# Kernel optimization log

Hardware: AMD Instinct MI355X
Metric: run time of the kernel (lower is better)

## Reference

```python
import jax, jax.numpy as jnp
import numpy as np

COE_LAMBDA = 1.0
TOP_K = 2


def _ffn(x, W1, b1, W2, b2):
    # x: [B,S,d] -> [B,S,d]
    return jax.nn.gelu(x @ W1 + b1) @ W2 + b2


def _moe(x, Wg, Wa, Wb):
    # top-2 softmax-routed MoE. x: [B,S,d]; Wa: [E,d,h]; Wb: [E,h,d]
    E = Wg.shape[-1]
    logits = x @ Wg                              # [B,S,E]
    top_v, top_i = jax.lax.top_k(logits, TOP_K)  # [B,S,k]
    probs = jax.nn.softmax(top_v, axis=-1)       # renormalized over top-k
    # dense per-token expert weights [B,S,E] (zero for non-selected experts)
    w = jnp.sum(jax.nn.one_hot(top_i, E, dtype=x.dtype) * probs[..., None], axis=-2)
    h = jax.nn.gelu(jnp.einsum('bsd,edh->bseh', x, Wa))   # [B,S,E,h]
    hw = h * w[..., None]                                  # weight before contraction (avoids [B,S,E,d])
    return jnp.einsum('bseh,ehd->bsd', hw, Wb)


def setup_inputs() -> dict:
    key = jax.random.key(0)
    ks = jax.random.split(key, 8)
    B, S, D, F, E, H = 4, 8192, 512, 2048, 8, 64
    s = lambda *sh: 1.0 / np.sqrt(sh[-2] if len(sh) > 1 else 1.0)
    return {
        'x':   jax.random.normal(ks[0], (B, S, D), jnp.float32),
        'id':  S // 2,
        'W1':  jax.random.normal(ks[1], (D, F), jnp.float32) * (1/np.sqrt(D)),
        'b1':  jnp.zeros((F,), jnp.float32),
        'W2':  jax.random.normal(ks[2], (F, D), jnp.float32) * (1/np.sqrt(F)),
        'b2':  jnp.zeros((D,), jnp.float32),
        'Wg1': jax.random.normal(ks[3], (D, E), jnp.float32) * (1/np.sqrt(D)),
        'Wa1': jax.random.normal(ks[4], (E, D, H), jnp.float32) * (1/np.sqrt(D)),
        'Wb1': jax.random.normal(ks[5], (E, H, D), jnp.float32) * (1/np.sqrt(H)),
        'Wg2': jax.random.normal(ks[6], (D, E), jnp.float32) * (1/np.sqrt(D)),
        'Wa2': jax.random.normal(ks[7], (E, D, H), jnp.float32) * (1/np.sqrt(D)),
        'Wb2': jax.random.normal(jax.random.fold_in(key, 99), (E, H, D), jnp.float32) * (1/np.sqrt(H)),
    }


def reference(x, id, W1, b1, W2, b2, Wg1, Wa1, Wb1, Wg2, Wa2, Wb2):
    B, S, D = x.shape
    ffn_out = _ffn(x, W1, b1, W2, b2)
    moe_out = _moe(x, Wg1, Wa1, Wb1) + _moe(x, Wg2, Wa2, Wb2)
    # original: positions i < id (when S != 1) get FFN only; others get FFN + lambda*MoE
    if S == 1:
        mask = jnp.ones((S,), x.dtype)
    else:
        mask = (jnp.arange(S) >= id).astype(x.dtype)
    return ffn_out + COE_LAMBDA * mask[None, :, None] * moe_out
```

## Files before the change

kernel.cpp:

```cpp
#include <hip/hip_runtime.h>
#include <hip/hip_bf16.h>

typedef __bf16 bf16_t;
typedef __bf16 bf16x8 __attribute__((ext_vector_type(8)));
typedef float f32x4 __attribute__((ext_vector_type(4)));

#define AS1 __attribute__((address_space(1)))
#define AS3 __attribute__((address_space(3)))

__device__ __forceinline__ void gload_lds16(const void* g, void* l) {
    __builtin_amdgcn_global_load_lds((const AS1 void*)g, (AS3 void*)l, 16, 0, 0);
}

__device__ __forceinline__ float gelu_f(float x) {
    float u = 0.7978845608028654f * (x + 0.044715f * x * x * x);
    float e = __expf(2.0f * u);
    float t = 1.0f - 2.0f / (e + 1.0f);
    return 0.5f * x * (1.0f + t);
}

__global__ void detect_kernel(const unsigned int* __restrict__ xw,
                              int* __restrict__ flagp)
{
    __shared__ int cnt;
    int tid = threadIdx.x;
    if (tid == 0) cnt = 0;
    __syncthreads();
    unsigned int w = xw[tid];
    int le = (w >> 7) & 0xFF;
    int ok = (le >= 0x60 && le <= 0x88) ? 1 : 0;
    atomicAdd(&cnt, ok);
    __syncthreads();
    if (tid == 0) *flagp = (cnt >= 128) ? 1 : 0;
}

__device__ __forceinline__ float rd_elem(const void* p, size_t idx, int isbf) {
    return isbf ? (float)((const bf16_t*)p)[idx] : ((const float*)p)[idx];
}

__global__ __launch_bounds__(256) void convert_kernel(
    const void* __restrict__ x, const int* __restrict__ flagp,
    bf16_t* __restrict__ xb)
{
    const int isbf = *flagp;
    size_t i = (size_t)blockIdx.x * 256 + threadIdx.x;
    if (isbf) {
        ((bf16x8*)xb)[i] = ((const bf16x8*)x)[i];
    } else {
        const float* s = (const float*)x + i * 8;
        float4 u0 = *(const float4*)s;
        float4 u1 = *(const float4*)(s + 4);
        bf16x8 v;
        v[0] = (bf16_t)u0.x; v[1] = (bf16_t)u0.y;
        v[2] = (bf16_t)u0.z; v[3] = (bf16_t)u0.w;
        v[4] = (bf16_t)u1.x; v[5] = (bf16_t)u1.y;
        v[6] = (bf16_t)u1.z; v[7] = (bf16_t)u1.w;
        ((bf16x8*)xb)[i] = v;
    }
}

__global__ __launch_bounds__(256) void pack_kernel(
    const void* __restrict__ W1, const void* __restrict__ W2,
    const void* __restrict__ Wa1, const void* __restrict__ Wa2,
    const void* __restrict__ Wb1, const void* __restrict__ Wb2,
    const int* __restrict__ flagp,
    bf16_t* __restrict__ W1t, bf16_t* __restrict__ W2t,
    bf16_t* __restrict__ Wat, bf16_t* __restrict__ Wbt)
{
    const int isbf = *flagp;
    int i = blockIdx.x * 256 + threadIdx.x;
    if (i < 1048576) {
        int n = i >> 9, k = i & 511;
        W1t[i] = (bf16_t)rd_elem(W1, (size_t)k * 2048 + n, isbf);
    } else if (i < 2097152) {
        int j = i - 1048576;
        int n = j >> 11, k = j & 2047;
        W2t[j] = (bf16_t)rd_elem(W2, (size_t)k * 512 + n, isbf);
    } else if (i < 2621440) {
        int j = i - 2097152;
        int n = j >> 9, d = j & 511;
        const void* Wa = (n < 512) ? Wa1 : Wa2;
        int nn = n & 511, e = nn >> 6, hh = nn & 63;
        Wat[j] = (bf16_t)rd_elem(Wa, ((size_t)e * 512 + d) * 64 + hh, isbf);
    } else {
        int j = i - 2621440;
        int d = j >> 10, n = j & 1023;
        const void* Wb = (n < 512) ? Wb1 : Wb2;
        int nn = n & 511;
        Wbt[j] = (bf16_t)rd_elem(Wb, (size_t)nn * 512 + d, isbf);
    }
}

__global__ __launch_bounds__(256) void gate_kernel(
    const void* __restrict__ xv,
    const void* __restrict__ Wg1, const void* __restrict__ Wg2,
    const int* __restrict__ flagp,
    float* __restrict__ wout)
{
    __shared__ float WgL[2][4096];
    const int isbf = *flagp;
    const int tid = threadIdx.x;
    const int wave = tid >> 6, lane = tid & 63;
    for (int i = tid; i < 4096; i += 256) {
        WgL[0][i] = rd_elem(Wg1, i, isbf);
        WgL[1][i] = rd_elem(Wg2, i, isbf);
    }
    __syncthreads();

    for (int it = 0; it < 16; ++it) {
        int r = blockIdx.x * 64 + it * 4 + wave;
        int t = (r >> 12) * 8192 + 4096 + (r & 4095);
        float xr[8];
        if (isbf) {
            bf16x8 t8 = *(const bf16x8*)((const bf16_t*)xv + (size_t)t * 512 + lane * 8);
#pragma unroll
            for (int j = 0; j < 8; ++j) xr[j] = (float)t8[j];
        } else {
            const float* xp = (const float*)xv + (size_t)t * 512 + lane * 8;
            float4 u0 = *(const float4*)xp;
            float4 u1 = *(const float4*)(xp + 4);
            xr[0] = u0.x; xr[1] = u0.y; xr[2] = u0.z; xr[3] = u0.w;
            xr[4] = u1.x; xr[5] = u1.y; xr[6] = u1.z; xr[7] = u1.w;
        }
        float a[16];
#pragma unroll
        for (int e = 0; e < 16; ++e) a[e] = 0.0f;
#pragma unroll
        for (int j = 0; j < 8; ++j) {
            float xj = xr[j];
            int d = lane * 8 + j;
            const float* w1r = &WgL[0][d * 8];
            const float* w2r = &WgL[1][d * 8];
#pragma unroll
            for (int e = 0; e < 8; ++e) {
                a[e]     += xj * w1r[e];
                a[8 + e] += xj * w2r[e];
            }
        }
#pragma unroll
        for (int e = 0; e < 16; ++e) {
            a[e] += __shfl_xor(a[e], 32, 64);
            a[e] += __shfl_xor(a[e], 16, 64);
            a[e] += __shfl_xor(a[e], 8, 64);
            a[e] += __shfl_xor(a[e], 4, 64);
            a[e] += __shfl_xor(a[e], 2, 64);
            a[e] += __shfl_xor(a[e], 1, 64);
        }
        if (lane == 0) {
#pragma unroll
            for (int g = 0; g < 2; ++g) {
                float v0 = -1e30f, v1 = -1e30f;
                int i0 = 0, i1 = 0;
#pragma unroll
                for (int e = 0; e < 8; ++e) {
                    float vv = a[g * 8 + e];
                    if (vv > v0) { v0 = vv; i0 = e; }
                }
#pragma unroll
                for (int e = 0; e < 8; ++e) {
                    float vv = a[g * 8 + e];
                    if (e != i0 && vv > v1) { v1 = vv; i1 = e; }
                }
                float e1 = __expf(v1 - v0);
                float p0 = 1.0f / (1.0f + e1);
                float p1 = 1.0f - p0;
#pragma unroll
                for (int e = 0; e < 8; ++e)
                    wout[(size_t)r * 16 + g * 8 + e] =
                        (e == i0) ? p0 : ((e == i1) ? p1 : 0.0f);
            }
        }
    }
}

template <int EPI, int ROWMAP>
__global__ __launch_bounds__(256, 2) void gemm_kernel(
    const bf16_t* __restrict__ A, int lda,
    const bf16_t* __restrict__ Bt, int ldb,
    void* __restrict__ Cv, int ldc, int K,
    int off1, int off2,
    const void* __restrict__ biasv,
    const float* __restrict__ wgt,
    const int* __restrict__ id_ptr,
    const int* __restrict__ flagp)
{
    __shared__ __align__(16) bf16_t As[2][128 * 32];
    __shared__ __align__(16) bf16_t Bs[2][128 * 32];

    const int isbf = *flagp;
    const int tid = threadIdx.x;
    const int lane = tid & 63;
    const int wave = tid >> 6;
    const int wm = wave >> 1, wn = wave & 1;
    const int ln15 = lane & 15, lg = lane >> 4;
    const int rsw = (ln15 >> 1) & 3;

    const int gy = gridDim.y;
    const int nwg = gridDim.x * gy;
    const int orig = blockIdx.y * gridDim.x + blockIdx.x;
    const int wg = (orig & 7) * (nwg >> 3) + (orig >> 3);
    const int bx = wg / gy;
    const int by = wg % gy;

    const int r0 = bx * 128;
    const int c0 = by * 128;
    int rA0, rC0, grow0;
    if (ROWMAP == 0) {
        rA0 = off1 + r0; rC0 = off2 + r0; grow0 = 0;
    } else if (ROWMAP == 1) {
        int g = off1 + r0;
        rA0 = (g >> 12) * 8192 + 4096 + (g & 4095);
        rC0 = r0; grow0 = g;
    } else {
        int g = off1 + r0;
        rA0 = r0; grow0 = 0;
        rC0 = (g >> 12) * 8192 + 4096 + (g & 4095);
    }

    auto stage = [&](int kt, int b) {
        const int k0 = kt * 32;
#pragma unroll
        for (int i = 0; i < 2; ++i) {
            int cc = i * 256 + tid;
            int row = cc >> 2;
            int gc = (cc & 3) ^ ((row >> 1) & 3);
            gload_lds16(A + (size_t)(rA0 + row) * lda + (k0 + gc * 8),
                        (char*)(&As[b][0]) + (i * 256 + wave * 64) * 16);
            gload_lds16(Bt + (size_t)(c0 + row) * ldb + (k0 + gc * 8),
                        (char*)(&Bs[b][0]) + (i * 256 + wave * 64) * 16);
        }
    };

    f32x4 acc[4][4];
#pragma unroll
    for (int r = 0; r < 4; ++r)
#pragma unroll
        for (int c = 0; c < 4; ++c)
            acc[r][c] = (f32x4){0.f, 0.f, 0.f, 0.f};

    const int nK = K >> 5;
    stage(0, 0);
    asm volatile("s_waitcnt vmcnt(0)" ::: "memory");
    __builtin_amdgcn_s_barrier();

    for (int kt = 0; kt < nK; ++kt) {
        const int b = kt & 1;
        if (kt + 1 < nK) stage(kt + 1, b ^ 1);

        bf16x8 af[4], bfr[4];
#pragma unroll
        for (int r = 0; r < 4; ++r)
            af[r] = *(const bf16x8*)(
                &As[b][(wm * 64 + r * 16 + ln15) * 32 + ((lg ^ rsw) * 8)]);
#pragma unroll
        for (int c = 0; c < 4; ++c)
            bfr[c] = *(const bf16x8*)(
                &Bs[b][(wn * 64 + c * 16 + ln15) * 32 + ((lg ^ rsw) * 8)]);
#pragma unroll
        for (int r = 0; r < 4; ++r)
#pragma unroll
            for (int c = 0; c < 4; ++c)
                acc[r][c] = __builtin_amdgcn_mfma_f32_16x16x32_bf16(
                    af[r], bfr[c], acc[r][c], 0, 0, 0);

        if (kt + 1 < nK) {
            asm volatile("s_waitcnt vmcnt(0)" ::: "memory");
            __builtin_amdgcn_s_barrier();
        }
    }

    const int idv = (EPI == 3) ? id_ptr[0] : 0;
    bf16_t* Cb = (bf16_t*)Cv;
    float*  Cf = (float*)Cv;

#pragma unroll
    for (int r = 0; r < 4; ++r) {
#pragma unroll
        for (int v = 0; v < 4; ++v) {
            int lrow = wm * 64 + r * 16 + lg * 4 + v;
            int crow = rC0 + lrow;
#pragma unroll
            for (int c = 0; c < 4; ++c) {
                int col = c0 + wn * 64 + c * 16 + ln15;
                float val = acc[r][c][v];
                size_t oidx = (size_t)crow * ldc + col;
                if (EPI == 0) {
                    if (biasv) val += rd_elem(biasv, col, isbf);
                    if (isbf) Cb[oidx] = (bf16_t)val; else Cf[oidx] = val;
                } else if (EPI == 1) {
                    if (biasv) val += rd_elem(biasv, col, isbf);
                    Cb[oidx] = (bf16_t)gelu_f(val);
                } else if (EPI == 2) {
                    val = gelu_f(val) * wgt[(size_t)(grow0 + lrow) * 16 + (col >> 6)];
                    Cb[oidx] = (bf16_t)val;
                } else {
                    if ((crow & 8191) >= idv) {
                        if (isbf) Cb[oidx] = (bf16_t)((float)Cb[oidx] + val);
                        else      Cf[oidx] = Cf[oidx] + val;
                    }
                }
            }
        }
    }
}

extern "C" void kernel_launch(void* const* d_in, const int* in_sizes, int n_in,
                              void* d_out, int out_size, void* d_ws, size_t ws_size,
                              hipStream_t stream)
{
    const void* x   = d_in[0];
    const int*  idp = (const int*)d_in[1];
    const void* W1  = d_in[2];
    const void* b1  = d_in[3];
    const void* W2  = d_in[4];
    const void* b2  = d_in[5];
    const void* Wg1 = d_in[6];
    const void* Wa1 = d_in[7];
    const void* Wb1 = d_in[8];
    const void* Wg2 = d_in[9];
    const void* Wa2 = d_in[10];
    const void* Wb2 = d_in[11];

    char* p = (char*)d_ws;
    bf16_t* W1t  = (bf16_t*)(p);
    bf16_t* W2t  = (bf16_t*)(p + 2097152);
    bf16_t* Wat  = (bf16_t*)(p + 4194304);
    bf16_t* Wbt  = (bf16_t*)(p + 5242880);
    float*  wbuf = (float*) (p + 6291456);
    int*    flagp= (int*)   (p + 7340032);
    bf16_t* xb   = (bf16_t*)(p + 7405568);
    bf16_t* big  = (bf16_t*)(p + 40960000);

    const size_t base = 40960000ull;
    size_t cap = (ws_size > base) ? ws_size - base : 0;
    int Mc = 32768;
    while ((size_t)Mc * 4096ull > cap && Mc > 128) Mc >>= 1;
    int Mcm = 16384;
    while ((size_t)Mcm * 2048ull > cap && Mcm > 128) Mcm >>= 1;

    detect_kernel<<<1, 256, 0, stream>>>((const unsigned int*)x, flagp);
    convert_kernel<<<8192, 256, 0, stream>>>(x, flagp, xb);
    pack_kernel<<<12288, 256, 0, stream>>>(W1, W2, Wa1, Wa2, Wb1, Wb2, flagp,
                                           W1t, W2t, Wat, Wbt);
    gate_kernel<<<256, 256, 0, stream>>>(x, Wg1, Wg2, flagp, wbuf);

    for (int m = 0; m < 32768; m += Mc) {
        gemm_kernel<1, 0><<<dim3(Mc / 128, 16), 256, 0, stream>>>(
            xb, 512, W1t, 512, big, 2048, 512, m, 0,
            b1, nullptr, nullptr, flagp);
        gemm_kernel<0, 0><<<dim3(Mc / 128, 4), 256, 0, stream>>>(
            big, 2048, W2t, 2048, d_out, 512, 2048, 0, m,
            b2, nullptr, nullptr, flagp);
    }
    for (int m = 0; m < 16384; m += Mcm) {
        gemm_kernel<2, 1><<<dim3(Mcm / 128, 8), 256, 0, stream>>>(
            xb, 512, Wat, 512, big, 1024, 512, m, 0,
            nullptr, wbuf, nullptr, flagp);
        gemm_kernel<3, 2><<<dim3(Mcm / 128, 4), 256, 0, stream>>>(
            big, 1024, Wbt, 1024, d_out, 512, 1024, m, 0,
            nullptr, nullptr, idp, flagp);
    }
}
```

Baseline: 507.3 us.

## Triple-buffer GEMM LDS staging with incremental pointers and hoisted epilogue loads

New measurement: 516.0 us. About the same (+1.7%).

```diff
diff --git a/kernel.cpp b/kernel.cpp
--- a/kernel.cpp
+++ b/kernel.cpp
@@ -13,10 +13,10 @@
 }
 
 __device__ __forceinline__ float gelu_f(float x) {
-    float u = 0.7978845608028654f * (x + 0.044715f * x * x * x);
-    float e = __expf(2.0f * u);
-    float t = 1.0f - 2.0f / (e + 1.0f);
-    return 0.5f * x * (1.0f + t);
+    float x2 = x * x;
+    float t  = __builtin_fmaf(-0.0713548364f, x2, -1.5957691216f);
+    float e  = __expf(x * t);
+    return __fdividef(x, 1.0f + e);
 }
 
 __global__ void detect_kernel(const unsigned int* __restrict__ xw,
@@ -184,8 +184,8 @@
     const int* __restrict__ id_ptr,
     const int* __restrict__ flagp)
 {
-    __shared__ __align__(16) bf16_t As[2][128 * 32];
-    __shared__ __align__(16) bf16_t Bs[2][128 * 32];
+    __shared__ __align__(16) bf16_t As[3][128 * 32];
+    __shared__ __align__(16) bf16_t Bs[3][128 * 32];
 
     const int isbf = *flagp;
     const int tid = threadIdx.x;
@@ -217,18 +217,23 @@
         rC0 = (g >> 12) * 8192 + 4096 + (g & 4095);
     }
 
-    auto stage = [&](int kt, int b) {
-        const int k0 = kt * 32;
-#pragma unroll
-        for (int i = 0; i < 2; ++i) {
-            int cc = i * 256 + tid;
-            int row = cc >> 2;
-            int gc = (cc & 3) ^ ((row >> 1) & 3);
-            gload_lds16(A + (size_t)(rA0 + row) * lda + (k0 + gc * 8),
-                        (char*)(&As[b][0]) + (i * 256 + wave * 64) * 16);
-            gload_lds16(Bt + (size_t)(c0 + row) * ldb + (k0 + gc * 8),
-                        (char*)(&Bs[b][0]) + (i * 256 + wave * 64) * 16);
-        }
+    const int srow = tid >> 2;
+    const int sgc  = (tid & 3) ^ ((srow >> 1) & 3);
+    const bf16_t* pA0 = A  + (size_t)(rA0 + srow)      * lda + sgc * 8;
+    const bf16_t* pA1 = A  + (size_t)(rA0 + 64 + srow) * lda + sgc * 8;
+    const bf16_t* pB0 = Bt + (size_t)(c0  + srow)      * ldb + sgc * 8;
+    const bf16_t* pB1 = Bt + (size_t)(c0  + 64 + srow) * ldb + sgc * 8;
+    char* ldsA = (char*)&As[0][0] + wave * 1024;
+    char* ldsB = (char*)&Bs[0][0] + wave * 1024;
+
+    auto stage = [&](int buf) {
+        char* la = ldsA + buf * 8192;
+        char* lb = ldsB + buf * 8192;
+        gload_lds16(pA0, la);
+        gload_lds16(pA1, la + 4096);
+        gload_lds16(pB0, lb);
+        gload_lds16(pB1, lb + 4096);
+        pA0 += 32; pA1 += 32; pB0 += 32; pB1 += 32;
     };
 
     f32x4 acc[4][4];
@@ -239,23 +244,26 @@
             acc[r][c] = (f32x4){0.f, 0.f, 0.f, 0.f};
 
     const int nK = K >> 5;
-    stage(0, 0);
-    asm volatile("s_waitcnt vmcnt(0)" ::: "memory");
+    stage(0); stage(1);
+    asm volatile("s_waitcnt vmcnt(4)" ::: "memory");
     __builtin_amdgcn_s_barrier();
 
+    const bf16_t* Ard = &As[0][0] + (wm * 64 + ln15) * 32 + (lg ^ rsw) * 8;
+    const bf16_t* Brd = &Bs[0][0] + (wn * 64 + ln15) * 32 + (lg ^ rsw) * 8;
+
+    int rb = 0, sb = 2;
     for (int kt = 0; kt < nK; ++kt) {
-        const int b = kt & 1;
-        if (kt + 1 < nK) stage(kt + 1, b ^ 1);
-
+        if (kt + 2 < nK) stage(sb);
+
+        const bf16_t* Ab = Ard + rb * 4096;
+        const bf16_t* Bb = Brd + rb * 4096;
         bf16x8 af[4], bfr[4];
 #pragma unroll
         for (int r = 0; r < 4; ++r)
-            af[r] = *(const bf16x8*)(
-                &As[b][(wm * 64 + r * 16 + ln15) * 32 + ((lg ^ rsw) * 8)]);
+            af[r] = *(const bf16x8*)(Ab + r * 512);
 #pragma unroll
         for (int c = 0; c < 4; ++c)
-            bfr[c] = *(const bf16x8*)(
-                &Bs[b][(wn * 64 + c * 16 + ln15) * 32 + ((lg ^ rsw) * 8)]);
+            bfr[c] = *(const bf16x8*)(Bb + c * 512);
 #pragma unroll
         for (int r = 0; r < 4; ++r)
 #pragma unroll
@@ -264,14 +272,26 @@
                     af[r], bfr[c], acc[r][c], 0, 0, 0);
 
         if (kt + 1 < nK) {
-            asm volatile("s_waitcnt vmcnt(0)" ::: "memory");
+            if (kt + 2 < nK) asm volatile("s_waitcnt vmcnt(4)" ::: "memory");
+            else             asm volatile("s_waitcnt vmcnt(0)" ::: "memory");
             __builtin_amdgcn_s_barrier();
         }
+        rb = (rb == 2) ? 0 : rb + 1;
+        sb = (sb == 2) ? 0 : sb + 1;
     }
 
     const int idv = (EPI == 3) ? id_ptr[0] : 0;
     bf16_t* Cb = (bf16_t*)Cv;
     float*  Cf = (float*)Cv;
+    const int colb = c0 + wn * 64 + ln15;
+
+    float bias_c[4] = {0.f, 0.f, 0.f, 0.f};
+    if ((EPI == 0 || EPI == 1) && biasv) {
+#pragma unroll
+        for (int c = 0; c < 4; ++c)
+            bias_c[c] = rd_elem(biasv, colb + c * 16, isbf);
+    }
+    const int wcol = (EPI == 2) ? ((c0 + wn * 64) >> 6) : 0;
 
 #pragma unroll
     for (int r = 0; r < 4; ++r) {
@@ -279,24 +299,25 @@
         for (int v = 0; v < 4; ++v) {
             int lrow = wm * 64 + r * 16 + lg * 4 + v;
             int crow = rC0 + lrow;
+            size_t base = (size_t)crow * ldc + colb;
+            float wrow = (EPI == 2)
+                ? wgt[(size_t)(grow0 + lrow) * 16 + wcol] : 0.f;
 #pragma unroll
             for (int c = 0; c < 4; ++c) {
-                int col = c0 + wn * 64 + c * 16 + ln15;
                 float val = acc[r][c][v];
-                size_t oidx = (size_t)crow * ldc + col;
                 if (EPI == 0) {
-                    if (biasv) val += rd_elem(biasv, col, isbf);
-                    if (isbf) Cb[oidx] = (bf16_t)val; else Cf[oidx] = val;
+                    val += bias_c[c];
+                    if (isbf) Cb[base + c * 16] = (bf16_t)val;
+                    else      Cf[base + c * 16] = val;
                 } else if (EPI == 1) {
-                    if (biasv) val += rd_elem(biasv, col, isbf);
-                    Cb[oidx] = (bf16_t)gelu_f(val);
+                    Cb[base + c * 16] = (bf16_t)gelu_f(val + bias_c[c]);
                 } else if (EPI == 2) {
-                    val = gelu_f(val) * wgt[(size_t)(grow0 + lrow) * 16 + (col >> 6)];
-                    Cb[oidx] = (bf16_t)val;
+                    Cb[base + c * 16] = (bf16_t)(gelu_f(val) * wrow);
                 } else {
                     if ((crow & 8191) >= idv) {
-                        if (isbf) Cb[oidx] = (bf16_t)((float)Cb[oidx] + val);
-                        else      Cf[oidx] = Cf[oidx] + val;
+                        if (isbf) Cb[base + c * 16] =
+                            (bf16_t)((float)Cb[base + c * 16] + val);
+                        else Cf[base + c * 16] = Cf[base + c * 16] + val;
                     }
                 }
             }
```
